# Performance work log

Hardware: AMD Instinct MI355X
Metric: run time of the kernel (lower is better)

The kernel has to match this reference:

```python
import jax, jax.numpy as jnp
import numpy as np

HEADS = 16
HEAD_DIM = 64
EMB = 1024
B, S = 4, 2048
SCALE = 1.0 / 8.0  # fixed constant in the original code
MASK_PENALTY = -50.0  # original adds -50 * upper_triangular, not -inf


def setup_inputs() -> dict:
    key = jax.random.key(0)
    ks = jax.random.split(key, 5)
    x = jax.random.normal(ks[0], (B, S, EMB), dtype=jnp.float32)
    Wq = jax.random.normal(ks[1], (EMB, HEADS * HEAD_DIM), dtype=jnp.float32) * 0.02
    Wk = jax.random.normal(ks[2], (EMB, HEADS * HEAD_DIM), dtype=jnp.float32) * 0.02
    Wv = jax.random.normal(ks[3], (EMB, HEADS * HEAD_DIM), dtype=jnp.float32) * 0.02
    Wr = jax.random.normal(ks[4], (HEADS * HEAD_DIM, EMB), dtype=jnp.float32) * 0.02
    return {"x": x, "Wq": Wq, "Wk": Wk, "Wv": Wv, "Wr": Wr}


def reference(x, Wq, Wk, Wv, Wr):
    b, s, _ = x.shape
    # project and split heads: [b, s, h, d]
    q = (x @ Wq).reshape(b, s, HEADS, HEAD_DIM)
    k = (x @ Wk).reshape(b, s, HEADS, HEAD_DIM)
    v = (x @ Wv).reshape(b, s, HEADS, HEAD_DIM)
    # scores: [b, h, s, s]
    scores = SCALE * jnp.einsum('bqhd,bkhd->bhqk', q, k)
    # causal additive mask: -50 on strictly-upper triangle (faithful to original)
    causal = jnp.triu(jnp.ones((s, s), dtype=x.dtype), k=1)
    scores = scores + MASK_PENALTY * causal
    attn = jax.nn.softmax(scores, axis=-1)
    out = jnp.einsum('bhqk,bkhd->bqhd', attn, v).reshape(b, s, HEADS * HEAD_DIM)
    return out @ Wr
```

## Files before the change

kernel.cpp:

```cpp
#include <hip/hip_runtime.h>

typedef _Float16 f16;
typedef _Float16 f16x8 __attribute__((ext_vector_type(8)));
typedef _Float16 f16x4 __attribute__((ext_vector_type(4)));
typedef float f32x4 __attribute__((ext_vector_type(4)));

#define MFMA16(A, B, C) __builtin_amdgcn_mfma_f32_16x16x32_f16((A), (B), (C), 0, 0, 0)

__device__ __forceinline__ void async16(void* lds, const void* gp) {
    __builtin_amdgcn_global_load_lds(
        (__attribute__((address_space(1))) void*)(gp),
        (__attribute__((address_space(3))) void*)(lds), 16, 0, 0);
}

__global__ __launch_bounds__(256) void k_prep(const float* __restrict__ x,
                                              const float* __restrict__ Wq,
                                              const float* __restrict__ Wk,
                                              const float* __restrict__ Wv,
                                              const float* __restrict__ Wr,
                                              f16* __restrict__ xb,
                                              f16* __restrict__ Wqkvt,
                                              f16* __restrict__ Wrt) {
    __shared__ float tile[32][33];
    int bid = blockIdx.x;
    if (bid < 8192) {
        int i = (bid * 256 + threadIdx.x) * 4;
        float4 v = *(const float4*)(x + i);
        f16x4 o = {(f16)v.x, (f16)v.y, (f16)v.z, (f16)v.w};
        *(f16x4*)(xb + i) = o;
    } else {
        int wid = bid - 8192;
        int z = wid >> 10;
        int tid = wid & 1023;
        const float* W = (z == 0) ? Wq : (z == 1) ? Wk : (z == 2) ? Wv : Wr;
        f16* Wt = (z == 3) ? Wrt : Wqkvt + z * 1048576;
        int c0 = (tid & 31) * 32, r0 = (tid >> 5) * 32;
        int tx = threadIdx.x & 31, ty = threadIdx.x >> 5;
#pragma unroll
        for (int j = 0; j < 32; j += 8)
            tile[ty + j][tx] = W[(r0 + ty + j) * 1024 + c0 + tx];
        __syncthreads();
#pragma unroll
        for (int j = 0; j < 32; j += 8)
            Wt[(c0 + ty + j) * 1024 + r0 + tx] = (f16)tile[tx][ty + j];
    }
}

__global__ __launch_bounds__(256) void k_transpose_v(const f16* __restrict__ QKV,
                                                     f16* __restrict__ Vt) {
    __shared__ f16 tile[32][33];
    int s0 = blockIdx.x * 32;
    int d0 = blockIdx.y * 32;
    int bh = blockIdx.z;
    int b = bh >> 4, h = bh & 15;
    int tx = threadIdx.x, ty = threadIdx.y;
#pragma unroll
    for (int j = 0; j < 32; j += 8)
        tile[ty + j][tx] = QKV[(b * 2048 + s0 + ty + j) * 3072 + 2048 + h * 64 + d0 + tx];
    __syncthreads();
#pragma unroll
    for (int j = 0; j < 32; j += 8)
        Vt[(bh * 64 + d0 + ty + j) * 2048 + s0 + tx] = tile[tx][ty + j];
}

template <bool OUT_F16>
__global__ __launch_bounds__(256) void k_gemm_bt(const f16* __restrict__ A,
                                                 const f16* __restrict__ Bt,
                                                 void* __restrict__ Cv,
                                                 int M, int N, int K) {
    __shared__ f16 As[2][128][32];
    __shared__ f16 Bs[2][128][32];
    int t = threadIdx.x;
    int lane = t & 63, w = t >> 6;
    int wm = (w >> 1) * 64, wn = (w & 1) * 64;
    int m0 = blockIdx.y * 128, n0 = blockIdx.x * 128;
    int ln = lane & 15, g = lane >> 4;

    int lin0 = w * 128 + lane, lin1 = lin0 + 64;
    int r0 = lin0 >> 2, c0 = (lin0 & 3) ^ ((r0 >> 1) & 3);
    int r1 = lin1 >> 2, c1 = (lin1 & 3) ^ ((r1 >> 1) & 3);
    const f16* gA0 = A + (size_t)(m0 + r0) * K + c0 * 8;
    const f16* gA1 = A + (size_t)(m0 + r1) * K + c1 * 8;
    const f16* gB0 = Bt + (size_t)(n0 + r0) * K + c0 * 8;
    const f16* gB1 = Bt + (size_t)(n0 + r1) * K + c1 * 8;

    f32x4 acc[4][4] = {};
    int sw = (ln >> 1) & 3;

#define GISSUE(bi, kk)                                    \
    do {                                                  \
        f16* lA = &As[bi][0][0] + w * 1024;               \
        f16* lB = &Bs[bi][0][0] + w * 1024;               \
        async16(lA, gA0 + (kk));                          \
        async16(lA + 512, gA1 + (kk));                    \
        async16(lB, gB0 + (kk));                          \
        async16(lB + 512, gB1 + (kk));                    \
    } while (0)

    GISSUE(0, 0);
    __syncthreads();

    int cur = 0;
    for (int k0 = 0; k0 < K; k0 += 32) {
        if (k0 + 32 < K) GISSUE(cur ^ 1, k0 + 32);
        f16x8 af[4], bf[4];
#pragma unroll
        for (int i = 0; i < 4; i++) {
            af[i] = *(const f16x8*)&As[cur][wm + i * 16 + ln][(g ^ sw) * 8];
            bf[i] = *(const f16x8*)&Bs[cur][wn + i * 16 + ln][(g ^ sw) * 8];
        }
#pragma unroll
        for (int mt = 0; mt < 4; mt++)
#pragma unroll
            for (int nt = 0; nt < 4; nt++)
                acc[mt][nt] = MFMA16(af[mt], bf[nt], acc[mt][nt]);
        __syncthreads();
        cur ^= 1;
    }
#undef GISSUE

    int rg = g * 4;
#pragma unroll
    for (int mt = 0; mt < 4; mt++)
#pragma unroll
        for (int nt = 0; nt < 4; nt++)
#pragma unroll
            for (int r = 0; r < 4; r++) {
                int row = m0 + wm + mt * 16 + rg + r;
                int col = n0 + wn + nt * 16 + ln;
                float v = acc[mt][nt][r];
                if (OUT_F16)
                    ((f16*)Cv)[(size_t)row * N + col] = (f16)v;
                else
                    ((float*)Cv)[(size_t)row * N + col] = v;
            }
}

__global__ __launch_bounds__(256, 2) void k_attn(const f16* __restrict__ QKV,
                                                 const f16* __restrict__ Vt,
                                                 f16* __restrict__ Opart,
                                                 float* __restrict__ Rsum) {
    __shared__ f16 Ks[2][64][64];
    __shared__ f16 Vs[2][64][64];
    int bh = blockIdx.x, pi = blockIdx.y;
    int b = bh >> 4, h = bh & 15;
    int t = threadIdx.x, lane = t & 63, wq = t >> 6;
    int ln = lane & 15, g = lane >> 4, g8 = g * 8, rg = g * 4;
    int sx = ln & 7;

    int r0 = wq * 8 + (lane >> 3);
    int cp = lane & 7;
    int cl = (cp ^ (r0 & 7)) * 8;
    int gk0 = ((r0 & 16) >> 2) | ((r0 & 12) << 1) | (r0 & 3);
    const f16* Kb = QKV + (size_t)b * 2048 * 3072 + 1024 + h * 64;
    const f16* Vb = Vt + (size_t)bh * 64 * 2048;
    const f16* gK0 = Kb + (size_t)gk0 * 3072 + cl;
    const f16* gK1 = Kb + (size_t)(gk0 + 32) * 3072 + cl;
    const f16* gV0 = Vb + (size_t)r0 * 2048 + cl;
    const f16* gV1 = Vb + (size_t)(r0 + 32) * 2048 + cl;

    const float C_SCL = 0.18033688f;
    const float C_MSK = -72.134752f;
    f16x8 ones;
#pragma unroll
    for (int j = 0; j < 8; j++) ones[j] = (f16)1.f;

    int nk0 = 16 - pi;

#define ISSUE(bi, j)                                                      \
    do {                                                                  \
        int jj = (j);                                                     \
        int kt_ = (jj < nk0) ? jj : jj - nk0 + pi + 1;                    \
        size_t kO = (size_t)kt_ * 64;                                     \
        async16(&Ks[bi][wq * 8][0],      gK0 + kO * 3072);                \
        async16(&Ks[bi][32 + wq * 8][0], gK1 + kO * 3072);                \
        async16(&Vs[bi][wq * 8][0],      gV0 + kO);                       \
        async16(&Vs[bi][32 + wq * 8][0], gV1 + kO);                       \
    } while (0)

    ISSUE(0, 0);
    __syncthreads();

    int i = 0;
    for (int phase = 0; phase < 2; phase++) {
        int qt  = phase ? pi : 15 - pi;
        int ktB = phase ? pi + 1 : 0;
        int ktE = phase ? 2 * pi + 2 : 16 - pi;
        int q0 = qt * 128;

        f16x8 bq[2][2];
#pragma unroll
        for (int nt = 0; nt < 2; nt++)
#pragma unroll
            for (int kd = 0; kd < 2; kd++)
                bq[nt][kd] = *(const f16x8*)(QKV +
                    (size_t)(b * 2048 + q0 + wq * 32 + nt * 16 + ln) * 3072 +
                    h * 64 + kd * 32 + g8);

        f32x4 oacc[2][4] = {};
        f32x4 osum[2] = {};

        for (int kt = ktB; kt < ktE; kt++, i++) {
            int cur = i & 1;
            int k0 = kt * 64;
            bool active = (k0 <= q0 + wq * 32 + 31);

            if (i + 1 < 17) ISSUE(cur ^ 1, i + 1);

            if (active) {
                f16x8 ak[2][4];
#pragma unroll
                for (int kd = 0; kd < 2; kd++)
#pragma unroll
                    for (int mt = 0; mt < 4; mt++)
                        ak[kd][mt] = *(const f16x8*)
                            &Ks[cur][mt * 16 + ln][((kd * 4 + g) ^ sx) * 8];
                f32x4 sacc[4][2] = {};
#pragma unroll
                for (int kd = 0; kd < 2; kd++)
#pragma unroll
                    for (int mt = 0; mt < 4; mt++)
#pragma unroll
                        for (int nt = 0; nt < 2; nt++)
                            sacc[mt][nt] = MFMA16(ak[kd][mt], bq[nt][kd], sacc[mt][nt]);

                bool needs_mask = (k0 + 63 > q0 + wq * 32);
                f16x8 ap[2][2];
#pragma unroll
                for (int nt = 0; nt < 2; nt++) {
                    int q = q0 + wq * 32 + nt * 16 + ln;
#pragma unroll
                    for (int mt = 0; mt < 4; mt++) {
                        int kb = mt >> 1, hi4 = (mt & 1) * 4;
#pragma unroll
                        for (int r = 0; r < 4; r++) {
                            float e;
                            if (needs_mask) {
                                int kk = k0 + kb * 32 + hi4 + 8 * g + r;
                                e = __builtin_amdgcn_exp2f(
                                    fmaf(sacc[mt][nt][r], C_SCL, (kk > q) ? C_MSK : 0.f));
                            } else {
                                e = __builtin_amdgcn_exp2f(sacc[mt][nt][r] * C_SCL);
                            }
                            ap[nt][kb][hi4 + r] = (f16)e;
                        }
                    }
                }

#pragma unroll
                for (int kk = 0; kk < 2; kk++) {
                    f16x8 bv[4];
#pragma unroll
                    for (int dt = 0; dt < 4; dt++)
                        bv[dt] = *(const f16x8*)
                            &Vs[cur][dt * 16 + ln][((kk * 4 + g) ^ sx) * 8];
#pragma unroll
                    for (int nt = 0; nt < 2; nt++) {
#pragma unroll
                        for (int dt = 0; dt < 4; dt++)
                            oacc[nt][dt] = MFMA16(ap[nt][kk], bv[dt], oacc[nt][dt]);
                        osum[nt] = MFMA16(ap[nt][kk], ones, osum[nt]);
                    }
                }
            }
            __syncthreads();
        }

        int u = (bh * 16 + qt) * 2 + phase;
#pragma unroll
        for (int nt = 0; nt < 2; nt++)
#pragma unroll
            for (int r = 0; r < 4; r++) {
                float rs = osum[nt][r];
                float inv = __builtin_amdgcn_rcpf(fmaxf(rs, 1e-30f));
                int q = wq * 32 + nt * 16 + rg + r;
                if (ln == 0) Rsum[u * 128 + q] = rs;
#pragma unroll
                for (int dt = 0; dt < 4; dt++)
                    Opart[(size_t)u * 8192 + q * 64 + dt * 16 + ln] =
                        (f16)(oacc[nt][dt][r] * inv);
            }
    }
#undef ISSUE
}

__global__ __launch_bounds__(256) void k_merge(const f16* __restrict__ Op,
                                               const float* __restrict__ Rs,
                                               f16* __restrict__ Ob) {
    int idx = blockIdx.x * 256 + threadIdx.x;
    int d8 = idx & 7;
    int q  = (idx >> 3) & 127;
    int qt = (idx >> 10) & 15;
    int bh = idx >> 14;
    int b = bh >> 4, hd = bh & 15;
    int u0 = (bh * 16 + qt) * 2;
    float rs0 = Rs[u0 * 128 + q], rs1 = Rs[(u0 + 1) * 128 + q];
    float inv = __builtin_amdgcn_rcpf(rs0 + rs1);
    f16x8 o0 = *(const f16x8*)(Op + (size_t)u0 * 8192 + q * 64 + d8 * 8);
    f16x8 o1 = *(const f16x8*)(Op + (size_t)(u0 + 1) * 8192 + q * 64 + d8 * 8);
    f16x8 o;
#pragma unroll
    for (int j = 0; j < 8; j++)
        o[j] = (f16)((rs0 * (float)o0[j] + rs1 * (float)o1[j]) * inv);
    *(f16x8*)(Ob + (size_t)(b * 2048 + qt * 128 + q) * 1024 + hd * 64 + d8 * 8) = o;
}

extern "C" void kernel_launch(void* const* d_in, const int* in_sizes, int n_in,
                              void* d_out, int out_size, void* d_ws, size_t ws_size,
                              hipStream_t stream) {
    const float* x = (const float*)d_in[0];
    const float* Wq = (const float*)d_in[1];
    const float* Wk = (const float*)d_in[2];
    const float* Wv = (const float*)d_in[3];
    const float* Wr = (const float*)d_in[4];
    float* out = (float*)d_out;

    f16* ws = (f16*)d_ws;
    f16* xb    = ws;
    f16* Wqkvt = xb + 8388608;
    f16* Wrt   = Wqkvt + 3145728;
    f16* QKVb  = Wrt + 1048576;
    f16* Vtb   = QKVb + 25165824;
    f16* Obuf  = Vtb + 8388608;
    f16* Opart = Obuf + 8388608;
    float* Rsum = (float*)(Opart + 16777216);

    k_prep<<<12288, 256, 0, stream>>>(x, Wq, Wk, Wv, Wr, xb, Wqkvt, Wrt);
    k_gemm_bt<true><<<dim3(24, 64), 256, 0, stream>>>(xb, Wqkvt, QKVb, 8192, 3072, 1024);
    dim3 tb(32, 8);
    k_transpose_v<<<dim3(64, 2, 64), tb, 0, stream>>>(QKVb, Vtb);
    k_attn<<<dim3(64, 16), 256, 0, stream>>>(QKVb, Vtb, Opart, Rsum);
    k_merge<<<4096, 256, 0, stream>>>(Opart, Rsum, Obuf);
    k_gemm_bt<false><<<dim3(8, 64), 256, 0, stream>>>(Obuf, Wrt, out, 8192, 1024, 1024);
}
```

Before: 272.5 us.

## Fuse all stages into one persistent cooperative kernel with grid syncs

```diff
diff --git a/kernel.cpp b/kernel.cpp
--- a/kernel.cpp
+++ b/kernel.cpp
@@ -1,4 +1,7 @@
 #include <hip/hip_runtime.h>
+#include <hip/hip_cooperative_groups.h>
+
+namespace cg = cooperative_groups;
 
 typedef _Float16 f16;
 typedef _Float16 f16x8 __attribute__((ext_vector_type(8)));
@@ -13,67 +16,21 @@
         (__attribute__((address_space(3))) void*)(lds), 16, 0, 0);
 }
 
-__global__ __launch_bounds__(256) void k_prep(const float* __restrict__ x,
-                                              const float* __restrict__ Wq,
-                                              const float* __restrict__ Wk,
-                                              const float* __restrict__ Wv,
-                                              const float* __restrict__ Wr,
-                                              f16* __restrict__ xb,
-                                              f16* __restrict__ Wqkvt,
-                                              f16* __restrict__ Wrt) {
-    __shared__ float tile[32][33];
-    int bid = blockIdx.x;
-    if (bid < 8192) {
-        int i = (bid * 256 + threadIdx.x) * 4;
-        float4 v = *(const float4*)(x + i);
-        f16x4 o = {(f16)v.x, (f16)v.y, (f16)v.z, (f16)v.w};
-        *(f16x4*)(xb + i) = o;
-    } else {
-        int wid = bid - 8192;
-        int z = wid >> 10;
-        int tid = wid & 1023;
-        const float* W = (z == 0) ? Wq : (z == 1) ? Wk : (z == 2) ? Wv : Wr;
-        f16* Wt = (z == 3) ? Wrt : Wqkvt + z * 1048576;
-        int c0 = (tid & 31) * 32, r0 = (tid >> 5) * 32;
-        int tx = threadIdx.x & 31, ty = threadIdx.x >> 5;
-#pragma unroll
-        for (int j = 0; j < 32; j += 8)
-            tile[ty + j][tx] = W[(r0 + ty + j) * 1024 + c0 + tx];
-        __syncthreads();
-#pragma unroll
-        for (int j = 0; j < 32; j += 8)
-            Wt[(c0 + ty + j) * 1024 + r0 + tx] = (f16)tile[tx][ty + j];
-    }
-}
-
-__global__ __launch_bounds__(256) void k_transpose_v(const f16* __restrict__ QKV,
-                                                     f16* __restrict__ Vt) {
-    __shared__ f16 tile[32][33];
-    int s0 = blockIdx.x * 32;
-    int d0 = blockIdx.y * 32;
-    int bh = blockIdx.z;
-    int b = bh >> 4, h = bh & 15;
-    int tx = threadIdx.x, ty = threadIdx.y;
-#pragma unroll
-    for (int j = 0; j < 32; j += 8)
-        tile[ty + j][tx] = QKV[(b * 2048 + s0 + ty + j) * 3072 + 2048 + h * 64 + d0 + tx];
-    __syncthreads();
-#pragma unroll
-    for (int j = 0; j < 32; j += 8)
-        Vt[(bh * 64 + d0 + ty + j) * 2048 + s0 + tx] = tile[tx][ty + j];
-}
+union SMem {
+    struct { f16 Ks[2 * 64 * 64]; f16 Vs[2 * 64 * 64]; } a;
+    struct { f16 As[2 * 128 * 32]; f16 Bs[2 * 128 * 32]; } g;
+    float wtile[32][33];
+    f16 vtile[32][33];
+};
 
 template <bool OUT_F16>
-__global__ __launch_bounds__(256) void k_gemm_bt(const f16* __restrict__ A,
-                                                 const f16* __restrict__ Bt,
-                                                 void* __restrict__ Cv,
-                                                 int M, int N, int K) {
-    __shared__ f16 As[2][128][32];
-    __shared__ f16 Bs[2][128][32];
-    int t = threadIdx.x;
+__device__ __forceinline__ void gemm_tile(const f16* __restrict__ A,
+                                          const f16* __restrict__ Bt,
+                                          void* __restrict__ Cv,
+                                          int N, int K, int m0, int n0,
+                                          f16* As, f16* Bs, int t) {
     int lane = t & 63, w = t >> 6;
     int wm = (w >> 1) * 64, wn = (w & 1) * 64;
-    int m0 = blockIdx.y * 128, n0 = blockIdx.x * 128;
     int ln = lane & 15, g = lane >> 4;
 
     int lin0 = w * 128 + lane, lin1 = lin0 + 64;
@@ -87,14 +44,14 @@
     f32x4 acc[4][4] = {};
     int sw = (ln >> 1) & 3;
 
-#define GISSUE(bi, kk)                                    \
-    do {                                                  \
-        f16* lA = &As[bi][0][0] + w * 1024;               \
-        f16* lB = &Bs[bi][0][0] + w * 1024;               \
-        async16(lA, gA0 + (kk));                          \
-        async16(lA + 512, gA1 + (kk));                    \
-        async16(lB, gB0 + (kk));                          \
-        async16(lB + 512, gB1 + (kk));                    \
+#define GISSUE(bi, kk)                                \
+    do {                                              \
+        f16* lA = As + (bi) * 4096 + w * 1024;        \
+        f16* lB = Bs + (bi) * 4096 + w * 1024;        \
+        async16(lA, gA0 + (kk));                      \
+        async16(lA + 512, gA1 + (kk));                \
+        async16(lB, gB0 + (kk));                      \
+        async16(lB + 512, gB1 + (kk));                \
     } while (0)
 
     GISSUE(0, 0);
@@ -106,8 +63,8 @@
         f16x8 af[4], bf[4];
 #pragma unroll
         for (int i = 0; i < 4; i++) {
-            af[i] = *(const f16x8*)&As[cur][wm + i * 16 + ln][(g ^ sw) * 8];
-            bf[i] = *(const f16x8*)&Bs[cur][wn + i * 16 + ln][(g ^ sw) * 8];
+            af[i] = *(const f16x8*)(As + cur * 4096 + (wm + i * 16 + ln) * 32 + (g ^ sw) * 8);
+            bf[i] = *(const f16x8*)(Bs + cur * 4096 + (wn + i * 16 + ln) * 32 + (g ^ sw) * 8);
         }
 #pragma unroll
         for (int mt = 0; mt < 4; mt++)
@@ -136,15 +93,13 @@
             }
 }
 
-__global__ __launch_bounds__(256, 2) void k_attn(const f16* __restrict__ QKV,
-                                                 const f16* __restrict__ Vt,
-                                                 f16* __restrict__ Opart,
-                                                 float* __restrict__ Rsum) {
-    __shared__ f16 Ks[2][64][64];
-    __shared__ f16 Vs[2][64][64];
-    int bh = blockIdx.x, pi = blockIdx.y;
+__device__ __forceinline__ void attn_unit(const f16* __restrict__ QKV,
+                                          const f16* __restrict__ Vt,
+                                          f16* __restrict__ Opart,
+                                          float* __restrict__ Rsum,
+                                          int bh, int pi, f16* Ks, f16* Vs, int t) {
     int b = bh >> 4, h = bh & 15;
-    int t = threadIdx.x, lane = t & 63, wq = t >> 6;
+    int lane = t & 63, wq = t >> 6;
     int ln = lane & 15, g = lane >> 4, g8 = g * 8, rg = g * 4;
     int sx = ln & 7;
 
@@ -172,10 +127,10 @@
         int jj = (j);                                                     \
         int kt_ = (jj < nk0) ? jj : jj - nk0 + pi + 1;                    \
         size_t kO = (size_t)kt_ * 64;                                     \
-        async16(&Ks[bi][wq * 8][0],      gK0 + kO * 3072);                \
-        async16(&Ks[bi][32 + wq * 8][0], gK1 + kO * 3072);                \
-        async16(&Vs[bi][wq * 8][0],      gV0 + kO);                       \
-        async16(&Vs[bi][32 + wq * 8][0], gV1 + kO);                       \
+        async16(Ks + (bi) * 4096 + wq * 512, gK0 + kO * 3072);            \
+        async16(Ks + (bi) * 4096 + 2048 + wq * 512, gK1 + kO * 3072);     \
+        async16(Vs + (bi) * 4096 + wq * 512, gV0 + kO);                   \
+        async16(Vs + (bi) * 4096 + 2048 + wq * 512, gV1 + kO);            \
     } while (0)
 
     ISSUE(0, 0);
@@ -213,8 +168,8 @@
                 for (int kd = 0; kd < 2; kd++)
 #pragma unroll
                     for (int mt = 0; mt < 4; mt++)
-                        ak[kd][mt] = *(const f16x8*)
-                            &Ks[cur][mt * 16 + ln][((kd * 4 + g) ^ sx) * 8];
+                        ak[kd][mt] = *(const f16x8*)(Ks + cur * 4096 +
+                            (mt * 16 + ln) * 64 + (((kd * 4 + g) ^ sx) * 8));
                 f32x4 sacc[4][2] = {};
 #pragma unroll
                 for (int kd = 0; kd < 2; kd++)
@@ -252,8 +207,8 @@
                     f16x8 bv[4];
 #pragma unroll
                     for (int dt = 0; dt < 4; dt++)
-                        bv[dt] = *(const f16x8*)
-                            &Vs[cur][dt * 16 + ln][((kk * 4 + g) ^ sx) * 8];
+                        bv[dt] = *(const f16x8*)(Vs + cur * 4096 +
+                            (dt * 16 + ln) * 64 + (((kk * 4 + g) ^ sx) * 8));
 #pragma unroll
                     for (int nt = 0; nt < 2; nt++) {
 #pragma unroll
@@ -284,25 +239,98 @@
 #undef ISSUE
 }
 
-__global__ __launch_bounds__(256) void k_merge(const f16* __restrict__ Op,
-                                               const float* __restrict__ Rs,
-                                               f16* __restrict__ Ob) {
-    int idx = blockIdx.x * 256 + threadIdx.x;
-    int d8 = idx & 7;
-    int q  = (idx >> 3) & 127;
-    int qt = (idx >> 10) & 15;
-    int bh = idx >> 14;
-    int b = bh >> 4, hd = bh & 15;
-    int u0 = (bh * 16 + qt) * 2;
-    float rs0 = Rs[u0 * 128 + q], rs1 = Rs[(u0 + 1) * 128 + q];
-    float inv = __builtin_amdgcn_rcpf(rs0 + rs1);
-    f16x8 o0 = *(const f16x8*)(Op + (size_t)u0 * 8192 + q * 64 + d8 * 8);
-    f16x8 o1 = *(const f16x8*)(Op + (size_t)(u0 + 1) * 8192 + q * 64 + d8 * 8);
-    f16x8 o;
-#pragma unroll
-    for (int j = 0; j < 8; j++)
-        o[j] = (f16)((rs0 * (float)o0[j] + rs1 * (float)o1[j]) * inv);
-    *(f16x8*)(Ob + (size_t)(b * 2048 + qt * 128 + q) * 1024 + hd * 64 + d8 * 8) = o;
+__global__ __launch_bounds__(256, 2) void k_mega(
+    const float* __restrict__ x, const float* __restrict__ Wq,
+    const float* __restrict__ Wk, const float* __restrict__ Wv,
+    const float* __restrict__ Wr, float* __restrict__ out,
+    f16* __restrict__ xb, f16* __restrict__ Wqkvt, f16* __restrict__ Wrt,
+    f16* __restrict__ QKVb, f16* __restrict__ Vtb, f16* __restrict__ Obuf,
+    f16* __restrict__ Opart, float* __restrict__ Rsum) {
+    __shared__ SMem sm;
+    cg::grid_group grid = cg::this_grid();
+    int t = threadIdx.x;
+
+    for (int vb = blockIdx.x; vb < 12288; vb += gridDim.x) {
+        if (vb < 8192) {
+            int i = (vb * 256 + t) * 4;
+            float4 v = *(const float4*)(x + i);
+            f16x4 o = {(f16)v.x, (f16)v.y, (f16)v.z, (f16)v.w};
+            *(f16x4*)(xb + i) = o;
+        } else {
+            int wid = vb - 8192;
+            int z = wid >> 10;
+            int tid = wid & 1023;
+            const float* W = (z == 0) ? Wq : (z == 1) ? Wk : (z == 2) ? Wv : Wr;
+            f16* Wt = (z == 3) ? Wrt : Wqkvt + z * 1048576;
+            int c0 = (tid & 31) * 32, rr0 = (tid >> 5) * 32;
+            int tx = t & 31, ty = t >> 5;
+#pragma unroll
+            for (int j = 0; j < 32; j += 8)
+                sm.wtile[ty + j][tx] = W[(rr0 + ty + j) * 1024 + c0 + tx];
+            __syncthreads();
+#pragma unroll
+            for (int j = 0; j < 32; j += 8)
+                Wt[(c0 + ty + j) * 1024 + rr0 + tx] = (f16)sm.wtile[tx][ty + j];
+            __syncthreads();
+        }
+    }
+    grid.sync();
+
+    for (int vt = blockIdx.x; vt < 1536; vt += gridDim.x) {
+        int n0 = (vt % 24) * 128;
+        int m0 = (vt / 24) * 128;
+        gemm_tile<true>(xb, Wqkvt, QKVb, 3072, 1024, m0, n0, sm.g.As, sm.g.Bs, t);
+    }
+    grid.sync();
+
+    for (int vb = blockIdx.x; vb < 8192; vb += gridDim.x) {
+        int s0 = (vb & 63) * 32;
+        int d0 = ((vb >> 6) & 1) * 32;
+        int bh = vb >> 7;
+        int b = bh >> 4, h = bh & 15;
+        int tx = t & 31, ty = t >> 5;
+#pragma unroll
+        for (int j = 0; j < 32; j += 8)
+            sm.vtile[ty + j][tx] =
+                QKVb[(b * 2048 + s0 + ty + j) * 3072 + 2048 + h * 64 + d0 + tx];
+        __syncthreads();
+#pragma unroll
+        for (int j = 0; j < 32; j += 8)
+            Vtb[(size_t)(bh * 64 + d0 + ty + j) * 2048 + s0 + tx] = sm.vtile[tx][ty + j];
+        __syncthreads();
+    }
+    grid.sync();
+
+    for (int vb = blockIdx.x; vb < 1024; vb += gridDim.x) {
+        attn_unit(QKVb, Vtb, Opart, Rsum, vb & 63, vb >> 6, sm.a.Ks, sm.a.Vs, t);
+    }
+    grid.sync();
+
+    for (int vb = blockIdx.x; vb < 4096; vb += gridDim.x) {
+        int idx = vb * 256 + t;
+        int d8 = idx & 7;
+        int q  = (idx >> 3) & 127;
+        int qt = (idx >> 10) & 15;
+        int bh = idx >> 14;
+        int b = bh >> 4, hd = bh & 15;
+        int u0 = (bh * 16 + qt) * 2;
+        float rs0 = Rsum[u0 * 128 + q], rs1 = Rsum[(u0 + 1) * 128 + q];
+        float inv = __builtin_amdgcn_rcpf(rs0 + rs1);
+        f16x8 o0 = *(const f16x8*)(Opart + (size_t)u0 * 8192 + q * 64 + d8 * 8);
+        f16x8 o1 = *(const f16x8*)(Opart + (size_t)(u0 + 1) * 8192 + q * 64 + d8 * 8);
+        f16x8 o;
+#pragma unroll
+        for (int j = 0; j < 8; j++)
+            o[j] = (f16)((rs0 * (float)o0[j] + rs1 * (float)o1[j]) * inv);
+        *(f16x8*)(Obuf + (size_t)(b * 2048 + qt * 128 + q) * 1024 + hd * 64 + d8 * 8) = o;
+    }
+    grid.sync();
+
+    for (int vt = blockIdx.x; vt < 512; vt += gridDim.x) {
+        int n0 = (vt % 8) * 128;
+        int m0 = (vt / 8) * 128;
+        gemm_tile<false>(Obuf, Wrt, out, 1024, 1024, m0, n0, sm.g.As, sm.g.Bs, t);
+    }
 }
 
 extern "C" void kernel_launch(void* const* d_in, const int* in_sizes, int n_in,
@@ -325,11 +353,16 @@
     f16* Opart = Obuf + 8388608;
     float* Rsum = (float*)(Opart + 16777216);
 
-    k_prep<<<12288, 256, 0, stream>>>(x, Wq, Wk, Wv, Wr, xb, Wqkvt, Wrt);
-    k_gemm_bt<true><<<dim3(24, 64), 256, 0, stream>>>(xb, Wqkvt, QKVb, 8192, 3072, 1024);
-    dim3 tb(32, 8);
-    k_transpose_v<<<dim3(64, 2, 64), tb, 0, stream>>>(QKVb, Vtb);
-    k_attn<<<dim3(64, 16), 256, 0, stream>>>(QKVb, Vtb, Opart, Rsum);
-    k_merge<<<4096, 256, 0, stream>>>(Opart, Rsum, Obuf);
-    k_gemm_bt<false><<<dim3(8, 64), 256, 0, stream>>>(Obuf, Wrt, out, 8192, 1024, 1024);
-}
+    static int nblk = 0;
+    if (nblk == 0) {
+        int bpc = 0;
+        hipOccupancyMaxActiveBlocksPerMultiprocessor(&bpc, k_mega, 256, 0);
+        if (bpc < 1) bpc = 1;
+        long cap = (long)bpc * 256;
+        nblk = (int)(cap < 1024 ? cap : 1024);
+    }
+
+    void* args[] = {&x, &Wq, &Wk, &Wv, &Wr, &out, &xb, &Wqkvt, &Wrt,
+                    &QKVb, &Vtb, &Obuf, &Opart, &Rsum};
+    hipLaunchCooperativeKernel((const void*)k_mega, dim3(nblk), dim3(256), args, 0, stream);
+}
```

Result: slower. 541.0 us (+98.5%).
